# Kernel tuning notes

Hardware: AMD Instinct MI355X
Metric: run time of the kernel (lower is better)

## Reference

```python
import jax, jax.numpy as jnp
import numpy as np

B, T = 16384, 64
VOCAB, D, HD, FF = 10, 3, 4, 2
EPS = 1e-6


def _rms(x, w):
    return x * jax.lax.rsqrt(jnp.mean(x * x, axis=-1, keepdims=True) + EPS) * w


def _rope(x, theta=3.0):
    # x: [..., T, HD]; interleaved rotary, matching the torch RotaryEmbedding
    t = jnp.arange(x.shape[-2], dtype=x.dtype)
    inv_freq = 1.0 / theta ** (jnp.arange(0, HD, 2, dtype=x.dtype) / HD)  # [HD/2]
    freqs = jnp.outer(t, inv_freq)                                        # [T, HD/2]
    cos_f, sin_f = jnp.cos(freqs), jnp.sin(freqs)
    x1, x2 = x[..., ::2], x[..., 1::2]
    rot = jnp.stack([x1 * cos_f - x2 * sin_f, x1 * sin_f + x2 * cos_f], axis=-1)
    return rot.reshape(x.shape)


def setup_inputs() -> dict:
    key = jax.random.key(0)
    ks = jax.random.split(key, 12)
    f32 = jnp.float32
    return {
        "idx": jax.random.randint(ks[0], (B, T), 0, VOCAB, dtype=jnp.int32),
        "arc_A": jnp.asarray(2.5, f32),
        "arc_start": jnp.asarray(-1.2, f32),
        "arc_stride": jnp.asarray(0.29, f32),
        "w_ln1": jnp.ones((D,), f32) + 0.1 * jax.random.normal(ks[1], (D,), f32),
        "w_ln2": jnp.ones((D,), f32) + 0.1 * jax.random.normal(ks[2], (D,), f32),
        "w_lnf": jnp.ones((D,), f32) + 0.1 * jax.random.normal(ks[3], (D,), f32),
        "w_qn": jnp.ones((HD,), f32) + 0.1 * jax.random.normal(ks[4], (HD,), f32),
        "Wq": jax.random.normal(ks[5], (HD, D), f32) * 0.5,
        "Wk": jax.random.normal(ks[6], (HD, D), f32) * 0.5,
        "Wg": jax.random.normal(ks[7], (FF, D), f32) * 0.5,
        "Wu": jax.random.normal(ks[8], (FF, D), f32) * 0.5,
        "Wd": jax.random.normal(ks[9], (D, FF), f32) * 0.5,
    }


def reference(idx, arc_A, arc_start, arc_stride, w_ln1, w_ln2, w_lnf, w_qn,
              Wq, Wk, Wg, Wu, Wd):
    dt = arc_A.dtype
    # circular-arc token embedding table [VOCAB, 2]
    digits = jnp.arange(VOCAB, dtype=dt)
    angles = arc_start + digits * arc_stride
    table = jnp.stack([arc_A * jnp.cos(angles), arc_A * jnp.sin(angles)], axis=1)

    tok = table[idx]                                              # [B,T,2]
    pe = jnp.sin(jnp.arange(T, dtype=dt) * jnp.exp(jnp.asarray(-np.log(10000.0), dt)))
    pos = jnp.broadcast_to(pe[None, :, None], (idx.shape[0], T, 1))
    x = jnp.concatenate([tok, pos], axis=-1)                      # [B,T,3]

    h = _rms(x, w_ln1)
    q = _rms(h @ Wq.T, w_qn)                                      # [B,T,HD]
    k = _rms(h @ Wk.T, w_qn)
    v = h @ Wk.T                                                  # v = k pre-norm? no: v = k.clone() BEFORE q_norm
    q = _rope(q)
    k = _rope(k)

    scale = HD ** (-0.5)
    scores = jnp.einsum("btd,bsd->bts", q, k) * scale             # [B,T,T]
    causal = jnp.triu(jnp.ones((T, T), dtype=bool), k=1)
    scores = jnp.where(causal, -jnp.inf, scores)
    attn = jax.nn.softmax(scores, axis=-1)
    out = jnp.einsum("bts,bsd->btd", attn, v)                     # [B,T,HD]

    x = x + out @ Wq                                              # F.linear(out, Wq.T) == out @ Wq
    h = _rms(x, w_ln2)
    x = x + (jax.nn.silu(h @ Wg.T) * (h @ Wu.T)) @ Wd.T
    x = _rms(x, w_lnf)
    return x[..., :2] @ table.T                                   # [B,T,VOCAB]
```

## Files before the change

kernel.cpp:

```cpp
#include <hip/hip_runtime.h>
#include <math.h>


namespace {
constexpr int kB = 16384;
constexpr int kT = 64;
constexpr int kVocab = 10;
constexpr float kEps = 1e-6f;
constexpr int kWaves = 4;

typedef float v2f __attribute__((ext_vector_type(2)));

__global__ __launch_bounds__(256, 6) void adder_model_kernel(
    const int* __restrict__ idx,
    const float* __restrict__ p_arcA,
    const float* __restrict__ p_arcStart,
    const float* __restrict__ p_arcStride,
    const float* __restrict__ w_ln1,
    const float* __restrict__ w_ln2,
    const float* __restrict__ w_lnf,
    const float* __restrict__ w_qn,
    const float* __restrict__ Wq,
    const float* __restrict__ Wk,
    const float* __restrict__ Wg,
    const float* __restrict__ Wu,
    const float* __restrict__ Wd,
    float* __restrict__ out)
{
    __shared__ float4 kArr[kWaves][kT];
    __shared__ float4 vArr[kWaves][kT];
    __shared__ float table_s[kVocab * 2];

    const int lane = threadIdx.x & 63;
    const int wid  = threadIdx.x >> 6;

    if (threadIdx.x < kVocab) {
        const float ang = p_arcStart[0] + (float)threadIdx.x * p_arcStride[0];
        const float A = p_arcA[0];
        table_s[2 * threadIdx.x]     = A * __cosf(ang);
        table_s[2 * threadIdx.x + 1] = A * __sinf(ang);
    }
    __syncthreads();

    float tb[2 * kVocab];
#pragma unroll
    for (int d = 0; d < 2 * kVocab; ++d) tb[d] = table_s[d];

    const float t_f = (float)lane;
    const float pe  = __sinf(t_f * 1e-4f);
    const float c0  = __cosf(t_f);
    const float s0  = __sinf(t_f);
    const float ang1 = t_f * 0.57735026918962576f;
    const float c1  = __cosf(ang1);
    const float s1  = __sinf(ang1);

    const float wl1_0 = w_ln1[0], wl1_1 = w_ln1[1], wl1_2 = w_ln1[2];
    const float wl2_0 = w_ln2[0], wl2_1 = w_ln2[1], wl2_2 = w_ln2[2];
    const float wlf0 = w_lnf[0], wlf1 = w_lnf[1];
    const float wqn0 = w_qn[0], wqn1 = w_qn[1], wqn2 = w_qn[2], wqn3 = w_qn[3];
    const float Wq00 = Wq[0],  Wq01 = Wq[1],  Wq02 = Wq[2];
    const float Wq10 = Wq[3],  Wq11 = Wq[4],  Wq12 = Wq[5];
    const float Wq20 = Wq[6],  Wq21 = Wq[7],  Wq22 = Wq[8];
    const float Wq30 = Wq[9],  Wq31 = Wq[10], Wq32 = Wq[11];
    const float Wk00 = Wk[0],  Wk01 = Wk[1],  Wk02 = Wk[2];
    const float Wk10 = Wk[3],  Wk11 = Wk[4],  Wk12 = Wk[5];
    const float Wk20 = Wk[6],  Wk21 = Wk[7],  Wk22 = Wk[8];
    const float Wk30 = Wk[9],  Wk31 = Wk[10], Wk32 = Wk[11];
    const float Wg00 = Wg[0],  Wg01 = Wg[1],  Wg02 = Wg[2];
    const float Wg10 = Wg[3],  Wg11 = Wg[4],  Wg12 = Wg[5];
    const float Wu00 = Wu[0],  Wu01 = Wu[1],  Wu02 = Wu[2];
    const float Wu10 = Wu[3],  Wu11 = Wu[4],  Wu12 = Wu[5];
    const float Wd00 = Wd[0],  Wd01 = Wd[1];
    const float Wd10 = Wd[2],  Wd11 = Wd[3];
    const float Wd20 = Wd[4],  Wd21 = Wd[5];

    const int row = (int)blockIdx.x * kWaves + wid;

    const int tix = idx[(size_t)row * kT + lane];
    const float x0i = table_s[2 * tix];
    const float x1i = table_s[2 * tix + 1];
    const float x2i = pe;

    const float r1 = __builtin_amdgcn_rsqf((x0i*x0i + x1i*x1i + x2i*x2i) * (1.0f/3.0f) + kEps);
    const float h0 = x0i * r1 * wl1_0;
    const float h1 = x1i * r1 * wl1_1;
    const float h2 = x2i * r1 * wl1_2;

    const float qp0 = h0*Wq00 + h1*Wq01 + h2*Wq02;
    const float qp1 = h0*Wq10 + h1*Wq11 + h2*Wq12;
    const float qp2 = h0*Wq20 + h1*Wq21 + h2*Wq22;
    const float qp3 = h0*Wq30 + h1*Wq31 + h2*Wq32;
    const float v0 = h0*Wk00 + h1*Wk01 + h2*Wk02;
    const float v1 = h0*Wk10 + h1*Wk11 + h2*Wk12;
    const float v2 = h0*Wk20 + h1*Wk21 + h2*Wk22;
    const float v3 = h0*Wk30 + h1*Wk31 + h2*Wk32;

    const float rq = __builtin_amdgcn_rsqf((qp0*qp0 + qp1*qp1 + qp2*qp2 + qp3*qp3) * 0.25f + kEps);
    const float rk = __builtin_amdgcn_rsqf((v0*v0 + v1*v1 + v2*v2 + v3*v3) * 0.25f + kEps);
    const float qn0 = qp0*rq*wqn0, qn1 = qp1*rq*wqn1, qn2 = qp2*rq*wqn2, qn3 = qp3*rq*wqn3;
    const float kn0 = v0*rk*wqn0,  kn1 = v1*rk*wqn1,  kn2 = v2*rk*wqn2,  kn3 = v3*rk*wqn3;

    constexpr float kQS = 0.72134752044448170f;
    const float q0 = (qn0*c0 - qn1*s0) * kQS;
    const float q1 = (qn0*s0 + qn1*c0) * kQS;
    const float q2 = (qn2*c1 - qn3*s1) * kQS;
    const float q3 = (qn2*s1 + qn3*c1) * kQS;
    const float k0 = kn0*c0 - kn1*s0;
    const float k1 = kn0*s0 + kn1*c0;
    const float k2 = kn2*c1 - kn3*s1;
    const float k3 = kn2*s1 + kn3*c1;

    kArr[wid][lane] = make_float4(k0, k1, k2, k3);
    vArr[wid][lane] = make_float4(v0, v1, v2, v3);
    __syncthreads();

    const v2f q01 = {q0, q1}, q23 = {q2, q3};
    v2f o01 = {0.0f, 0.0f}, o23 = {0.0f, 0.0f};
    float l = 0.0f;
    const float4* __restrict__ kp = kArr[wid];
    const float4* __restrict__ vp = vArr[wid];
#pragma unroll
    for (int s = 0; s < kT; ++s) {
        const float4 kk = kp[s];
        const float4 vv = vp[s];
        v2f p = q01 * v2f{kk.x, kk.y} + q23 * v2f{kk.z, kk.w};
        float sc = p.x + p.y;
        sc = (s <= lane) ? sc : -INFINITY;
        const float e = __builtin_amdgcn_exp2f(sc);
        l += e;
        const v2f e2 = {e, e};
        o01 += e2 * v2f{vv.x, vv.y};
        o23 += e2 * v2f{vv.z, vv.w};
    }

    const float invl = __builtin_amdgcn_rcpf(l);
    const float o0 = o01.x * invl, o1 = o01.y * invl;
    const float o2 = o23.x * invl, o3 = o23.y * invl;

    const float xa0 = x0i + o0*Wq00 + o1*Wq10 + o2*Wq20 + o3*Wq30;
    const float xa1 = x1i + o0*Wq01 + o1*Wq11 + o2*Wq21 + o3*Wq31;
    const float xa2 = x2i + o0*Wq02 + o1*Wq12 + o2*Wq22 + o3*Wq32;

    const float r2 = __builtin_amdgcn_rsqf((xa0*xa0 + xa1*xa1 + xa2*xa2) * (1.0f/3.0f) + kEps);
    const float hh0 = xa0*r2*wl2_0, hh1 = xa1*r2*wl2_1, hh2 = xa2*r2*wl2_2;
    const float g0 = hh0*Wg00 + hh1*Wg01 + hh2*Wg02;
    const float g1 = hh0*Wg10 + hh1*Wg11 + hh2*Wg12;
    const float u0 = hh0*Wu00 + hh1*Wu01 + hh2*Wu02;
    const float u1 = hh0*Wu10 + hh1*Wu11 + hh2*Wu12;
    constexpr float kL2E = 1.4426950408889634f;
    const float f0 = g0 * __builtin_amdgcn_rcpf(1.0f + __builtin_amdgcn_exp2f(-g0 * kL2E)) * u0;
    const float f1 = g1 * __builtin_amdgcn_rcpf(1.0f + __builtin_amdgcn_exp2f(-g1 * kL2E)) * u1;
    const float xf0 = xa0 + f0*Wd00 + f1*Wd01;
    const float xf1 = xa1 + f0*Wd10 + f1*Wd11;
    const float xf2 = xa2 + f0*Wd20 + f1*Wd21;

    const float rf = __builtin_amdgcn_rsqf((xf0*xf0 + xf1*xf1 + xf2*xf2) * (1.0f/3.0f) + kEps);
    const float y0 = xf0 * rf * wlf0;
    const float y1 = xf1 * rf * wlf1;

    float2* op = (float2*)(out + (size_t)(row * kT + lane) * kVocab);
#pragma unroll
    for (int d = 0; d < kVocab / 2; ++d) {
        float2 o2v;
        o2v.x = y0 * tb[4*d]     + y1 * tb[4*d + 1];
        o2v.y = y0 * tb[4*d + 2] + y1 * tb[4*d + 3];
        op[d] = o2v;
    }
}
}

extern "C" void kernel_launch(void* const* d_in, const int* in_sizes, int n_in,
                              void* d_out, int out_size, void* d_ws, size_t ws_size,
                              hipStream_t stream) {
    (void)in_sizes; (void)n_in; (void)d_ws; (void)ws_size; (void)out_size;
    const int*   idx       = (const int*)  d_in[0];
    const float* arcA      = (const float*)d_in[1];
    const float* arcStart  = (const float*)d_in[2];
    const float* arcStride = (const float*)d_in[3];
    const float* w_ln1     = (const float*)d_in[4];
    const float* w_ln2     = (const float*)d_in[5];
    const float* w_lnf     = (const float*)d_in[6];
    const float* w_qn      = (const float*)d_in[7];
    const float* Wq        = (const float*)d_in[8];
    const float* Wk        = (const float*)d_in[9];
    const float* Wg        = (const float*)d_in[10];
    const float* Wu        = (const float*)d_in[11];
    const float* Wd        = (const float*)d_in[12];
    float* out = (float*)d_out;

    dim3 grid(4096), block(256);
    hipLaunchKernelGGL(adder_model_kernel, grid, block, 0, stream,
                       idx, arcA, arcStart, arcStride,
                       w_ln1, w_ln2, w_lnf, w_qn, Wq, Wk, Wg, Wu, Wd, out);
}
```

Baseline: 113.8 us.

## Compute causal attention with bf16 MFMA using split-precision Q/K and LDS staging

Replaces the per-lane scalar 64-step attention loop with 32x32x16 bf16 MFMA tiles. Q and K are split into high and low bf16 parts so scores keep near-fp32 accuracy, and the upper-triangular tile is skipped. Exponentiated scores and V (with an extra ones row that yields the softmax denominator) go through per-wave LDS buffers. This adds bf16 rounding of P and V, larger LDS use that lowers occupancy (launch bounds drop from 6 to 3), and relies on wave-local __threadfence_block in place of block barriers.

```diff
diff --git a/kernel.cpp b/kernel.cpp
--- a/kernel.cpp
+++ b/kernel.cpp
@@ -3,15 +3,67 @@
 
 
 namespace {
-constexpr int kB = 16384;
-constexpr int kT = 64;
 constexpr int kVocab = 10;
 constexpr float kEps = 1e-6f;
 constexpr int kWaves = 4;
 
-typedef float v2f __attribute__((ext_vector_type(2)));
-
-__global__ __launch_bounds__(256, 6) void adder_model_kernel(
+typedef __attribute__((ext_vector_type(8)))  short short8;
+typedef __attribute__((ext_vector_type(16))) float float16;
+
+constexpr int kOffQh  = 0;
+constexpr int kOffQl  = 512;
+constexpr int kOffKh  = 1024;
+constexpr int kOffKl  = 1536;
+constexpr int kOffO   = 0;
+constexpr int kOffP   = 2048;
+constexpr int kOffVt  = 11264;
+constexpr int kWaveLds = 12544;
+constexpr int kPP = 72;
+constexpr int kOP = 76;
+
+__device__ __forceinline__ unsigned bf16_rn(float x) {
+    const unsigned u = __float_as_uint(x);
+    return (u + 0x7fffu + ((u >> 16) & 1u)) >> 16;
+}
+__device__ __forceinline__ unsigned pk_bf16(float a, float b) {
+    return bf16_rn(a) | (bf16_rn(b) << 16);
+}
+__device__ __forceinline__ float bf_lo(unsigned u) { return __uint_as_float(u << 16); }
+__device__ __forceinline__ float bf_hi(unsigned u) { return __uint_as_float(u & 0xffff0000u); }
+
+__device__ __forceinline__ float16 mfma(short8 a, short8 b, float16 c) {
+    return __builtin_amdgcn_mfma_f32_32x32x16_bf16(a, b, c, 0, 0, 0);
+}
+
+__device__ __forceinline__ short8 tok_frag(const char* wbase, int off, int tok, bool lo_half) {
+    uint2 r = *(const uint2*)(wbase + off + tok * 8);
+    uint4 t;
+    t.x = lo_half ? r.x : 0u;
+    t.y = lo_half ? r.y : 0u;
+    t.z = 0u; t.w = 0u;
+    return __builtin_bit_cast(short8, t);
+}
+
+template<int TM, int TN, bool MASKED>
+__device__ __forceinline__ void exp_store(const float16& S, ushort* P, int tloc, int h, int m) {
+    const int t = TN * 32 + tloc;
+#pragma unroll
+    for (int c = 0; c < 4; ++c) {
+        float e[4];
+#pragma unroll
+        for (int j = 0; j < 4; ++j) {
+            float sc = S[4 * c + j];
+            if (MASKED) sc = ((j + 8 * c) <= m) ? sc : -INFINITY;
+            e[j] = __builtin_amdgcn_exp2f(sc);
+        }
+        uint2 w;
+        w.x = pk_bf16(e[0], e[1]);
+        w.y = pk_bf16(e[2], e[3]);
+        *(uint2*)(P + t * kPP + TM * 32 + 8 * c + 4 * h) = w;
+    }
+}
+
+__global__ __launch_bounds__(256, 3) void adder_model_kernel(
     const int* __restrict__ idx,
     const float* __restrict__ p_arcA,
     const float* __restrict__ p_arcStart,
@@ -27,12 +79,12 @@
     const float* __restrict__ Wd,
     float* __restrict__ out)
 {
-    __shared__ float4 kArr[kWaves][kT];
-    __shared__ float4 vArr[kWaves][kT];
+    __shared__ __align__(16) char smem[kWaves][kWaveLds];
     __shared__ float table_s[kVocab * 2];
 
     const int lane = threadIdx.x & 63;
     const int wid  = threadIdx.x >> 6;
+    char* wbase = &smem[wid][0];
 
     if (threadIdx.x < kVocab) {
         const float ang = p_arcStart[0] + (float)threadIdx.x * p_arcStride[0];
@@ -76,7 +128,7 @@
 
     const int row = (int)blockIdx.x * kWaves + wid;
 
-    const int tix = idx[(size_t)row * kT + lane];
+    const int tix = idx[(size_t)row * 64 + lane];
     const float x0i = table_s[2 * tix];
     const float x1i = table_s[2 * tix + 1];
     const float x2i = pe;
@@ -110,32 +162,91 @@
     const float k2 = kn2*c1 - kn3*s1;
     const float k3 = kn2*s1 + kn3*c1;
 
-    kArr[wid][lane] = make_float4(k0, k1, k2, k3);
-    vArr[wid][lane] = make_float4(v0, v1, v2, v3);
-    __syncthreads();
-
-    const v2f q01 = {q0, q1}, q23 = {q2, q3};
-    v2f o01 = {0.0f, 0.0f}, o23 = {0.0f, 0.0f};
-    float l = 0.0f;
-    const float4* __restrict__ kp = kArr[wid];
-    const float4* __restrict__ vp = vArr[wid];
-#pragma unroll
-    for (int s = 0; s < kT; ++s) {
-        const float4 kk = kp[s];
-        const float4 vv = vp[s];
-        v2f p = q01 * v2f{kk.x, kk.y} + q23 * v2f{kk.z, kk.w};
-        float sc = p.x + p.y;
-        sc = (s <= lane) ? sc : -INFINITY;
-        const float e = __builtin_amdgcn_exp2f(sc);
-        l += e;
-        const v2f e2 = {e, e};
-        o01 += e2 * v2f{vv.x, vv.y};
-        o23 += e2 * v2f{vv.z, vv.w};
-    }
-
-    const float invl = __builtin_amdgcn_rcpf(l);
-    const float o0 = o01.x * invl, o1 = o01.y * invl;
-    const float o2 = o23.x * invl, o3 = o23.y * invl;
+    uint2 qh, ql, kh, kl;
+    qh.x = pk_bf16(q0, q1); qh.y = pk_bf16(q2, q3);
+    ql.x = pk_bf16(q0 - bf_lo(qh.x), q1 - bf_hi(qh.x));
+    ql.y = pk_bf16(q2 - bf_lo(qh.y), q3 - bf_hi(qh.y));
+    kh.x = pk_bf16(k0, k1); kh.y = pk_bf16(k2, k3);
+    kl.x = pk_bf16(k0 - bf_lo(kh.x), k1 - bf_hi(kh.x));
+    kl.y = pk_bf16(k2 - bf_lo(kh.y), k3 - bf_hi(kh.y));
+    *(uint2*)(wbase + kOffQh + lane * 8) = qh;
+    *(uint2*)(wbase + kOffQl + lane * 8) = ql;
+    *(uint2*)(wbase + kOffKh + lane * 8) = kh;
+    *(uint2*)(wbase + kOffKl + lane * 8) = kl;
+
+    ushort* Vt = (ushort*)(wbase + kOffVt);
+    Vt[0 * kPP + lane] = (ushort)bf16_rn(v0);
+    Vt[1 * kPP + lane] = (ushort)bf16_rn(v1);
+    Vt[2 * kPP + lane] = (ushort)bf16_rn(v2);
+    Vt[3 * kPP + lane] = (ushort)bf16_rn(v3);
+    Vt[4 * kPP + lane] = 0x3F80;
+    __threadfence_block();
+
+    const int tloc = lane & 31;
+    const bool loh = lane < 32;
+    const int h    = lane >> 5;
+    const int m    = tloc - 4 * h;
+
+    const short8 aKh0 = tok_frag(wbase, kOffKh, tloc,      loh);
+    const short8 aKl0 = tok_frag(wbase, kOffKl, tloc,      loh);
+    const short8 aKh1 = tok_frag(wbase, kOffKh, tloc + 32, loh);
+    const short8 aKl1 = tok_frag(wbase, kOffKl, tloc + 32, loh);
+    const short8 bQh0 = tok_frag(wbase, kOffQh, tloc,      loh);
+    const short8 bQl0 = tok_frag(wbase, kOffQl, tloc,      loh);
+    const short8 bQh1 = tok_frag(wbase, kOffQh, tloc + 32, loh);
+    const short8 bQl1 = tok_frag(wbase, kOffQl, tloc + 32, loh);
+
+    float16 Z = {0,0,0,0,0,0,0,0,0,0,0,0,0,0,0,0};
+    float16 S00 = mfma(aKl0, bQh0, mfma(aKh0, bQl0, mfma(aKh0, bQh0, Z)));
+    float16 S01 = mfma(aKl0, bQh1, mfma(aKh0, bQl1, mfma(aKh0, bQh1, Z)));
+    float16 S11 = mfma(aKl1, bQh1, mfma(aKh1, bQl1, mfma(aKh1, bQh1, Z)));
+
+    ushort* P = (ushort*)(wbase + kOffP);
+    exp_store<0, 0, true >(S00, P, tloc, h, m);
+    exp_store<0, 1, false>(S01, P, tloc, h, m);
+    exp_store<1, 1, true >(S11, P, tloc, h, m);
+    __threadfence_block();
+
+    short8 vb[4];
+#pragma unroll
+    for (int kc = 0; kc < 4; ++kc)
+        vb[kc] = __builtin_bit_cast(short8,
+            *(const uint4*)(Vt + (tloc & 7) * kPP + 16 * kc + 8 * h));
+
+    float16 acc0 = Z, acc1 = Z;
+#pragma unroll
+    for (int kc = 0; kc < 2; ++kc) {
+        short8 pa = __builtin_bit_cast(short8,
+            *(const uint4*)(P + tloc * kPP + 16 * kc + 8 * h));
+        acc0 = mfma(pa, vb[kc], acc0);
+    }
+#pragma unroll
+    for (int kc = 0; kc < 4; ++kc) {
+        short8 pa = __builtin_bit_cast(short8,
+            *(const uint4*)(P + (tloc + 32) * kPP + 16 * kc + 8 * h));
+        acc1 = mfma(pa, vb[kc], acc1);
+    }
+
+    float* Ol = (float*)(wbase + kOffO);
+    if (tloc < 5) {
+#pragma unroll
+        for (int c = 0; c < 4; ++c) {
+            float4 w0 = make_float4(acc0[4*c], acc0[4*c+1], acc0[4*c+2], acc0[4*c+3]);
+            *(float4*)(Ol + tloc * kOP +      8 * c + 4 * h) = w0;
+            float4 w1 = make_float4(acc1[4*c], acc1[4*c+1], acc1[4*c+2], acc1[4*c+3]);
+            *(float4*)(Ol + tloc * kOP + 32 + 8 * c + 4 * h) = w1;
+        }
+    }
+    __threadfence_block();
+
+    const float o0r = Ol[0 * kOP + lane];
+    const float o1r = Ol[1 * kOP + lane];
+    const float o2r = Ol[2 * kOP + lane];
+    const float o3r = Ol[3 * kOP + lane];
+    const float lr  = Ol[4 * kOP + lane];
+
+    const float invl = __builtin_amdgcn_rcpf(lr);
+    const float o0 = o0r * invl, o1 = o1r * invl, o2 = o2r * invl, o3 = o3r * invl;
 
     const float xa0 = x0i + o0*Wq00 + o1*Wq10 + o2*Wq20 + o3*Wq30;
     const float xa1 = x1i + o0*Wq01 + o1*Wq11 + o2*Wq21 + o3*Wq31;
@@ -158,7 +269,7 @@
     const float y0 = xf0 * rf * wlf0;
     const float y1 = xf1 * rf * wlf1;
 
-    float2* op = (float2*)(out + (size_t)(row * kT + lane) * kVocab);
+    float2* op = (float2*)(out + (size_t)(row * 64 + lane) * kVocab);
 #pragma unroll
     for (int d = 0; d < kVocab / 2; ++d) {
         float2 o2v;
```

Measured after the change: 112.8 us. About the same (-0.9%).
